# Kernel optimization log

Hardware: AMD Instinct MI355X
Metric: run time of the kernel (lower is better)

## Reference

```python
import jax, jax.numpy as jnp
import numpy as np
import math

C, HEADS = 128, 4
HD = C // HEADS
MID = max(C // 4, 8)

def _conv1x1(x, W, b):
    # x: (B?, C, H, W) ; W: (O, C) ; b: (O,)
    return jnp.einsum('bchw,oc->bohw', x, W) + b[None, :, None, None]

def _conv3x3(x, W, b):
    # W: (O, I, 3, 3), NCHW / OIHW, SAME padding
    y = jax.lax.conv_general_dilated(x, W, window_strides=(1, 1), padding='SAME',
                                     dimension_numbers=('NCHW', 'OIHW', 'NCHW'))
    return y + b[None, :, None, None]

def setup_inputs() -> dict:
    key = jax.random.key(0)
    ks = jax.random.split(key, 24)
    B, N, H, W = 4, 6, 128, 128
    s = 0.05
    inp = {
        'bev_views': jax.random.normal(ks[0], (B, N, C, H, W), jnp.float32),
        'snr_db': jax.random.normal(ks[1], (B, 1), jnp.float32) * 10.0,
        'view_reliability': jax.random.uniform(ks[2], (B, N, 3), jnp.float32),
        'Wq': jax.random.normal(ks[3], (C, C), jnp.float32) * s,
        'bq': jnp.zeros((C,), jnp.float32),
        'Wk': jax.random.normal(ks[4], (C, C), jnp.float32) * s,
        'bk': jnp.zeros((C,), jnp.float32),
        'Wv': jax.random.normal(ks[5], (C, C), jnp.float32) * s,
        'bv': jnp.zeros((C,), jnp.float32),
        'Wo1': jax.random.normal(ks[6], (C, C), jnp.float32) * s,
        'bo1': jnp.zeros((C,), jnp.float32),
        'Wo2': jax.random.normal(ks[7], (C, C, 3, 3), jnp.float32) * s,
        'bo2': jnp.zeros((C,), jnp.float32),
        'Wc1': jax.random.normal(ks[8], (MID, C), jnp.float32) * s,
        'bc1': jnp.zeros((MID,), jnp.float32),
        'Wc2': jax.random.normal(ks[9], (1, MID), jnp.float32) * s,
        'bc2': jnp.zeros((1,), jnp.float32),
        'Wg': jax.random.normal(ks[10], (C, 1), jnp.float32) * s,
        'bg': jnp.zeros((C,), jnp.float32),
        'Wr1': jax.random.normal(ks[11], (MID, 3), jnp.float32) * s,
        'br1': jnp.zeros((MID,), jnp.float32),
        'Wr2': jax.random.normal(ks[12], (1, MID), jnp.float32) * s,
        'br2': jnp.zeros((1,), jnp.float32),
    }
    return inp

def reference(bev_views, snr_db, view_reliability,
              Wq, bq, Wk, bk, Wv, bv, Wo1, bo1, Wo2, bo2,
              Wc1, bc1, Wc2, bc2, Wg, bg, Wr1, br1, Wr2, br2):
    B, N, Cc, H, W = bev_views.shape
    # --- cross-view semantic denoising (per-pixel cross-view attention) ---
    gq = bev_views.mean(axis=1)                       # (B,C,H,W)
    q = _conv1x1(gq, Wq, bq).reshape(B, HEADS, HD, H, W)
    flat = bev_views.reshape(B * N, Cc, H, W)
    k = _conv1x1(flat, Wk, bk).reshape(B, N, HEADS, HD, H, W)
    v = _conv1x1(flat, Wv, bv).reshape(B, N, HEADS, HD, H, W)
    # score over head_dim, softmax over views N
    score = jnp.einsum('bmdhw,bnmdhw->bnmhw', q, k) / math.sqrt(HD)
    attn = jax.nn.softmax(score, axis=1)              # (B,N,heads,H,W)
    fused = jnp.einsum('bnmhw,bnmdhw->bmdhw', attn, v).reshape(B, Cc, H, W)
    fused = _conv3x3(jax.nn.relu(_conv1x1(fused, Wo1, bo1)), Wo2, bo2) + gq
    attn_map = attn.mean(axis=2)                      # (B,N,H,W)
    # --- confidence-gated fusion ---
    conf = _conv1x1(jax.nn.relu(_conv1x1(flat, Wc1, bc1)), Wc2, bc2)
    conf_logits = conf.reshape(B, N, 1, H, W)
    rel_bias = (jax.nn.relu(view_reliability.reshape(B * N, 3) @ Wr1.T + br1) @ Wr2.T + br2)
    conf_logits = conf_logits + rel_bias.reshape(B, N, 1, 1, 1)
    conf_weights = jax.nn.softmax(conf_logits, axis=1)  # (B,N,1,H,W)
    fused_conf = (conf_weights * bev_views).sum(axis=1)  # (B,C,H,W)
    # --- SNR gate ---
    snr_norm = jnp.clip(snr_db / 20.0, -1.5, 1.5)       # (B,1)
    gate = jax.nn.sigmoid(snr_norm @ Wg.T + bg).reshape(B, Cc, 1, 1)
    out = gate * fused + (1.0 - gate) * fused_conf
    return (out, attn_map, conf_weights)
```

## Files before the change

### kernel.cpp

```cpp
#include <hip/hip_runtime.h>
#include <hip/hip_bf16.h>
#include <math.h>


#define BB   4
#define NV   6
#define CH   128
#define HGT  128
#define WID  128
#define MIDD 32
#define HWP  (HGT*WID)
#define TP   32

#define SWZ(pix) (((pix) & 15) << 3)

typedef __attribute__((ext_vector_type(8))) short bf16x8;
typedef __attribute__((ext_vector_type(4))) float f32x4;
typedef __attribute__((ext_vector_type(2))) unsigned int u32x2;

union U8 { bf16x8 v; unsigned u[4]; };

__device__ __forceinline__ ushort f2bf(float f) {
    union { __hip_bfloat16 h; ushort u; } v;
    v.h = __float2bfloat16(f);
    return v.u;
}
__device__ __forceinline__ float bf2f(ushort u) {
    return __uint_as_float(((unsigned)u) << 16);
}
__device__ __forceinline__ unsigned cvt_pk_bf16(float lo, float hi) {
    unsigned r;
    asm("v_cvt_pk_bf16_f32 %0, %1, %2" : "=v"(r) : "v"(lo), "v"(hi));
    return r;
}

__global__ void fusion_setup(const float* __restrict__ snr, const float* __restrict__ vr,
                             const float* __restrict__ Wg, const float* __restrict__ bg,
                             const float* __restrict__ Wr1, const float* __restrict__ br1,
                             const float* __restrict__ Wr2, const float* __restrict__ br2,
                             float* __restrict__ relb, float* __restrict__ gate)
{
    int tid = blockIdx.x * blockDim.x + threadIdx.x;
    if (tid < BB*CH) {
        int b = tid >> 7, c = tid & 127;
        float s = snr[b] * 0.05f;
        s = fminf(fmaxf(s, -1.5f), 1.5f);
        float z = s * Wg[c] + bg[c];
        gate[tid] = 1.0f / (1.0f + __expf(-z));
    }
    if (tid < BB*NV) {
        int b = tid / NV, n = tid % NV;
        float v0 = vr[(b*NV+n)*3+0], v1 = vr[(b*NV+n)*3+1], v2 = vr[(b*NV+n)*3+2];
        float acc = br2[0];
        for (int j = 0; j < MIDD; ++j) {
            float h = Wr1[j*3+0]*v0 + Wr1[j*3+1]*v1 + Wr1[j*3+2]*v2 + br1[j];
            acc += Wr2[j] * fmaxf(h, 0.0f);
        }
        relb[tid] = acc;
    }
}

__global__ void pack_weights(const float* __restrict__ Wq, const float* __restrict__ Wk,
                             const float* __restrict__ Wv, const float* __restrict__ Wo1,
                             const float* __restrict__ Wc1, const float* __restrict__ Wo2,
                             ushort* __restrict__ wqp, ushort* __restrict__ wkp,
                             ushort* __restrict__ wvp, ushort* __restrict__ wo1p,
                             ushort* __restrict__ wc1p, ushort* __restrict__ wo2p)
{
    int tid = blockIdx.x * 256 + threadIdx.x;
    if (tid >= 27136) return;
    if (tid < 8192) {
        int m = tid >> 11;
        int local = tid & 2047;
        const float* src = (m == 0) ? Wq : (m == 1) ? Wk : (m == 2) ? Wv : Wo1;
        ushort* dst = (m == 0) ? wqp : (m == 1) ? wkp : (m == 2) ? wvp : wo1p;
        int ks = local >> 9, rem = local & 511;
        int nf = rem >> 6, lane = rem & 63;
        int o = nf*16 + (lane & 15);
        int i0 = ks*32 + ((lane >> 4) << 3);
        const float* s = src + o*CH + i0;
        ushort* d = dst + local*8;
#pragma unroll
        for (int j = 0; j < 8; ++j) d[j] = f2bf(s[j]);
    } else if (tid < 8704) {
        int local = tid - 8192;
        int ks = local >> 7, rem = local & 127;
        int nf = rem >> 6, lane = rem & 63;
        int o = nf*16 + (lane & 15);
        int i0 = ks*32 + ((lane >> 4) << 3);
        const float* s = Wc1 + o*CH + i0;
        ushort* d = wc1p + local*8;
#pragma unroll
        for (int j = 0; j < 8; ++j) d[j] = f2bf(s[j]);
    } else {
        int l2 = tid - 8704;
        int lane = l2 & 63;
        int rest = l2 >> 6;
        int nf = rest & 7;
        int kst = rest >> 3;
        int ks = kst & 3;
        int tap = kst >> 2;
        int co = nf*16 + (lane & 15);
        int ci0 = ks*32 + ((lane >> 4) << 3);
        ushort* d = wo2p + l2*8;
#pragma unroll
        for (int j = 0; j < 8; ++j) d[j] = f2bf(Wo2[(co*CH + ci0 + j)*9 + tap]);
    }
}

__device__ __forceinline__ bf16x8 ldsA(const ushort* tile, int lane, int mf, int ks) {
    int pix = mf*16 + (lane & 15);
    int idx = (pix*128 + ks*32 + ((lane >> 4) << 3)) ^ SWZ(pix);
    return *(const bf16x8*)(tile + idx);
}
__device__ __forceinline__ bf16x8 ldB(const ushort* pack, int lane, int ks, int nf, int NF) {
    return *(const bf16x8*)(pack + (((ks*NF + nf)*64) + lane)*8);
}

__global__ __launch_bounds__(256, 3) void fusion_attn(
    const float* __restrict__ bev,
    const ushort* __restrict__ wqp, const ushort* __restrict__ wkp,
    const ushort* __restrict__ wvp, const ushort* __restrict__ wo1p,
    const ushort* __restrict__ wc1p,
    const float* __restrict__ bq, const float* __restrict__ bk,
    const float* __restrict__ bv, const float* __restrict__ bo1,
    const float* __restrict__ bc1, const float* __restrict__ bc2,
    const float* __restrict__ Wc2, const float* __restrict__ relb,
    ushort* __restrict__ gq_bf, ushort* __restrict__ t_bf, ushort* __restrict__ fc_bf,
    float* __restrict__ attn_o, float* __restrict__ conf_o)
{
    __shared__ ushort xt[NV][TP*128];
    __shared__ float  scat[NV][4][TP];
    __shared__ float  dnm[4][TP];
    __shared__ float  lpart[NV][TP];
    __shared__ float  cfw[NV][TP];

    const int t = threadIdx.x, lane = t & 63, w = t >> 6;
    const int vb = ((blockIdx.x & 7) << 8) | (blockIdx.x >> 3);
    const int b = vb >> 9;
    const int pix0 = (vb & 511) * TP;

    const int pixg = (t & 3) * 8;
    const int c0   = (t >> 2) * 2;
    const float* sb = bev + (((size_t)b*NV*CH + c0)*HWP + pix0 + pixg);
    const size_t vstep = (size_t)CH*HWP;
    float gacc[16];
#pragma unroll
    for (int i = 0; i < 16; ++i) gacc[i] = 0.f;
    float4 L[NV][4];
#pragma unroll
    for (int j = 0; j < NV; ++j) {
        const float* s1 = sb + (size_t)j*vstep;
        L[j][0] = *(const float4*)(s1);
        L[j][1] = *(const float4*)(s1 + 4);
        L[j][2] = *(const float4*)(s1 + HWP);
        L[j][3] = *(const float4*)(s1 + HWP + 4);
    }
#pragma unroll
    for (int n = 0; n < NV; ++n) {
        float4 a0 = L[n][0], a1 = L[n][1], b0 = L[n][2], b1 = L[n][3];
        float r0[8] = {a0.x,a0.y,a0.z,a0.w, a1.x,a1.y,a1.z,a1.w};
        float r1[8] = {b0.x,b0.y,b0.z,b0.w, b1.x,b1.y,b1.z,b1.w};
#pragma unroll
        for (int p = 0; p < 8; ++p) {
            int pix = pixg + p;
            unsigned pk = cvt_pk_bf16(r0[p], r1[p]);
            *(unsigned*)(&xt[n][(pix*128 + c0) ^ SWZ(pix)]) = pk;
            gacc[p]   += r0[p];
            gacc[8+p] += r1[p];
        }
    }
    {
        U8 g0, g1;
#pragma unroll
        for (int p = 0; p < 4; ++p) {
            g0.u[p] = cvt_pk_bf16(gacc[2*p]   * (1.0f/6.0f), gacc[2*p+1] * (1.0f/6.0f));
            g1.u[p] = cvt_pk_bf16(gacc[8+2*p] * (1.0f/6.0f), gacc[9+2*p] * (1.0f/6.0f));
        }
        ushort* gd = gq_bf + ((size_t)(b*CH + c0)*HWP + pix0 + pixg);
        *(bf16x8*)(gd)       = g0.v;
        *(bf16x8*)(gd + HWP) = g1.v;
    }
    __syncthreads();

    const int cl0 = (lane & 15);
    const int rg  = (lane >> 4) << 2;

    f32x4 qf[2][2];
#pragma unroll
    for (int mf = 0; mf < 2; ++mf)
#pragma unroll
        for (int nfl = 0; nfl < 2; ++nfl) qf[mf][nfl] = (f32x4){0.f,0.f,0.f,0.f};
#pragma unroll 2
    for (int n = 0; n < NV; ++n) {
        bf16x8 xA[2][4];
#pragma unroll
        for (int mf = 0; mf < 2; ++mf)
#pragma unroll
            for (int ks = 0; ks < 4; ++ks) xA[mf][ks] = ldsA(xt[n], lane, mf, ks);
#pragma unroll
        for (int nfl = 0; nfl < 2; ++nfl) {
#pragma unroll
            for (int ks = 0; ks < 4; ++ks) {
                bf16x8 bb = ldB(wqp, lane, ks, 2*w + nfl, 8);
#pragma unroll
                for (int mf = 0; mf < 2; ++mf)
                    qf[mf][nfl] = __builtin_amdgcn_mfma_f32_16x16x32_bf16(bb, xA[mf][ks], qf[mf][nfl], 0, 0, 0);
            }
        }
        if (n == w || n == w + 4) {
            f32x4 cf[2][2];
#pragma unroll
            for (int mf = 0; mf < 2; ++mf)
#pragma unroll
                for (int nfc = 0; nfc < 2; ++nfc) cf[mf][nfc] = (f32x4){0.f,0.f,0.f,0.f};
#pragma unroll
            for (int nfc = 0; nfc < 2; ++nfc) {
#pragma unroll
                for (int ks = 0; ks < 4; ++ks) {
                    bf16x8 bb = ldB(wc1p, lane, ks, nfc, 2);
#pragma unroll
                    for (int mf = 0; mf < 2; ++mf)
                        cf[mf][nfc] = __builtin_amdgcn_mfma_f32_16x16x32_bf16(bb, xA[mf][ks], cf[mf][nfc], 0, 0, 0);
                }
            }
            const f32x4 bc1T0 = *(const f32x4*)(bc1 + rg),  bc1T1 = *(const f32x4*)(bc1 + 16 + rg);
            const f32x4 wc2T0 = *(const f32x4*)(Wc2 + rg),  wc2T1 = *(const f32x4*)(Wc2 + 16 + rg);
#pragma unroll
            for (int mf = 0; mf < 2; ++mf) {
                float pl = 0.f;
#pragma unroll
                for (int r = 0; r < 4; ++r) {
                    pl += fmaxf(cf[mf][0][r] + bc1T0[r], 0.f) * wc2T0[r];
                    pl += fmaxf(cf[mf][1][r] + bc1T1[r], 0.f) * wc2T1[r];
                }
                pl += __shfl_xor(pl, 16, 64);
                pl += __shfl_xor(pl, 32, 64);
                if (lane < 16) lpart[n][mf*16 + lane] = pl;
            }
        }
    }
    {
        const f32x4 bqT0 = *(const f32x4*)(bq + w*32 + rg), bqT1 = *(const f32x4*)(bq + w*32 + 16 + rg);
#pragma unroll
        for (int mf = 0; mf < 2; ++mf)
#pragma unroll
            for (int r = 0; r < 4; ++r) {
                qf[mf][0][r] = qf[mf][0][r]*(1.0f/6.0f) + bqT0[r];
                qf[mf][1][r] = qf[mf][1][r]*(1.0f/6.0f) + bqT1[r];
            }
    }

    float sb2[2];
    {
        const f32x4 bkT0 = *(const f32x4*)(bk + w*32 + rg), bkT1 = *(const f32x4*)(bk + w*32 + 16 + rg);
#pragma unroll
        for (int mf = 0; mf < 2; ++mf) {
            float v = 0.f;
#pragma unroll
            for (int r = 0; r < 4; ++r) {
                v += qf[mf][0][r]*bkT0[r];
                v += qf[mf][1][r]*bkT1[r];
            }
            sb2[mf] = v;
        }
    }
    float denom[2] = {0.f, 0.f};
#pragma unroll 2
    for (int n = 0; n < NV; ++n) {
        bf16x8 xA[2][4];
#pragma unroll
        for (int mf = 0; mf < 2; ++mf)
#pragma unroll
            for (int ks = 0; ks < 4; ++ks) xA[mf][ks] = ldsA(xt[n], lane, mf, ks);
        f32x4 kf[2][2];
#pragma unroll
        for (int mf = 0; mf < 2; ++mf)
#pragma unroll
            for (int nfl = 0; nfl < 2; ++nfl) kf[mf][nfl] = (f32x4){0.f,0.f,0.f,0.f};
#pragma unroll
        for (int nfl = 0; nfl < 2; ++nfl)
#pragma unroll
            for (int ks = 0; ks < 4; ++ks) {
                bf16x8 bb = ldB(wkp, lane, ks, 2*w + nfl, 8);
#pragma unroll
                for (int mf = 0; mf < 2; ++mf)
                    kf[mf][nfl] = __builtin_amdgcn_mfma_f32_16x16x32_bf16(bb, xA[mf][ks], kf[mf][nfl], 0, 0, 0);
            }
#pragma unroll
        for (int mf = 0; mf < 2; ++mf) {
            float s = sb2[mf];
#pragma unroll
            for (int r = 0; r < 4; ++r) {
                s += qf[mf][0][r]*kf[mf][0][r];
                s += qf[mf][1][r]*kf[mf][1][r];
            }
            s += __shfl_xor(s, 16, 64);
            s += __shfl_xor(s, 32, 64);
            float e = __expf(s * 0.17677669529663687f);
            denom[mf] += e;
            if (lane < 16) scat[n][w][mf*16 + lane] = e;
        }
    }
    const float inv0 = 1.0f/denom[0], inv1 = 1.0f/denom[1];
    if (lane < 32) dnm[w][lane] = (lane & 16) ? inv1 : inv0;

    f32x4 ff[2][2];
#pragma unroll
    for (int mf = 0; mf < 2; ++mf)
#pragma unroll
        for (int nfl = 0; nfl < 2; ++nfl) ff[mf][nfl] = (f32x4){0.f,0.f,0.f,0.f};
#pragma unroll 2
    for (int n = 0; n < NV; ++n) {
        bf16x8 xA[2][4];
#pragma unroll
        for (int mf = 0; mf < 2; ++mf)
#pragma unroll
            for (int ks = 0; ks < 4; ++ks) xA[mf][ks] = ldsA(xt[n], lane, mf, ks);
        f32x4 vv[2][2];
#pragma unroll
        for (int mf = 0; mf < 2; ++mf)
#pragma unroll
            for (int nfl = 0; nfl < 2; ++nfl) vv[mf][nfl] = (f32x4){0.f,0.f,0.f,0.f};
#pragma unroll
        for (int nfl = 0; nfl < 2; ++nfl)
#pragma unroll
            for (int ks = 0; ks < 4; ++ks) {
                bf16x8 bb = ldB(wvp, lane, ks, 2*w + nfl, 8);
#pragma unroll
                for (int mf = 0; mf < 2; ++mf)
                    vv[mf][nfl] = __builtin_amdgcn_mfma_f32_16x16x32_bf16(bb, xA[mf][ks], vv[mf][nfl], 0, 0, 0);
            }
        float a0 = scat[n][w][cl0]      * inv0;
        float a1 = scat[n][w][16 + cl0] * inv1;
#pragma unroll
        for (int r = 0; r < 4; ++r) {
            ff[0][0][r] += a0 * vv[0][0][r];
            ff[0][1][r] += a0 * vv[0][1][r];
            ff[1][0][r] += a1 * vv[1][0][r];
            ff[1][1][r] += a1 * vv[1][1][r];
        }
    }
    {
        const f32x4 bvT0 = *(const f32x4*)(bv + w*32 + rg), bvT1 = *(const f32x4*)(bv + w*32 + 16 + rg);
#pragma unroll
        for (int mf = 0; mf < 2; ++mf)
#pragma unroll
            for (int r = 0; r < 4; ++r) { ff[mf][0][r] += bvT0[r]; ff[mf][1][r] += bvT1[r]; }
    }
    __syncthreads();

    if (t < 32) {
        int pix = t;
        float bc2v = bc2[0];
        float lg[NV];
#pragma unroll
        for (int n = 0; n < NV; ++n)
            lg[n] = lpart[n][pix] + bc2v + relb[b*NV + n];
        float mx = fmaxf(fmaxf(fmaxf(lg[0],lg[1]),fmaxf(lg[2],lg[3])),fmaxf(lg[4],lg[5]));
        float e[NV], sum = 0.f;
#pragma unroll
        for (int n = 0; n < NV; ++n) { e[n] = __expf(lg[n]-mx); sum += e[n]; }
        float inv = 1.0f/sum;
#pragma unroll
        for (int n = 0; n < NV; ++n) {
            float wv = e[n]*inv;
            cfw[n][pix] = wv;
            conf_o[(b*NV + n)*HWP + pix0 + pix] = wv;
        }
    }
    if (t < 192) {
        int n = t >> 5, pix = t & 31;
        float am = 0.25f*(scat[n][0][pix]*dnm[0][pix] + scat[n][1][pix]*dnm[1][pix]
                        + scat[n][2][pix]*dnm[2][pix] + scat[n][3][pix]*dnm[3][pix]);
        attn_o[(b*NV + n)*HWP + pix0 + pix] = am;
    }
    __syncthreads();

    {
        float fcv[16];
#pragma unroll
        for (int i = 0; i < 16; ++i) fcv[i] = 0.f;
#pragma unroll
        for (int n = 0; n < NV; ++n) {
#pragma unroll
            for (int p = 0; p < 8; ++p) {
                int pix = pixg + p;
                float cwv = cfw[n][pix];
                unsigned pk = *(const unsigned*)(&xt[n][(pix*128 + c0) ^ SWZ(pix)]);
                fcv[p]   += cwv * bf2f((ushort)(pk & 0xffffu));
                fcv[8+p] += cwv * bf2f((ushort)(pk >> 16));
            }
        }
        U8 f0, f1;
#pragma unroll
        for (int p = 0; p < 4; ++p) {
            f0.u[p] = cvt_pk_bf16(fcv[2*p],   fcv[2*p+1]);
            f1.u[p] = cvt_pk_bf16(fcv[8+2*p], fcv[9+2*p]);
        }
        ushort* fd = fc_bf + ((size_t)(b*CH + c0)*HWP + pix0 + pixg);
        *(bf16x8*)(fd)       = f0.v;
        *(bf16x8*)(fd + HWP) = f1.v;
    }
    __syncthreads();

    {
        ushort* xt0 = &xt[0][0];
#pragma unroll
        for (int mf = 0; mf < 2; ++mf)
#pragma unroll
            for (int nfl = 0; nfl < 2; ++nfl) {
                int pix = mf*16 + cl0;
                int c   = w*32 + nfl*16 + rg;
                unsigned lo = cvt_pk_bf16(ff[mf][nfl][0], ff[mf][nfl][1]);
                unsigned hi = cvt_pk_bf16(ff[mf][nfl][2], ff[mf][nfl][3]);
                *(u32x2*)(&xt0[(pix*128 + c) ^ SWZ(pix)]) = (u32x2){lo, hi};
            }
    }
    __syncthreads();

    {
        bf16x8 aA[2][4];
#pragma unroll
        for (int mf = 0; mf < 2; ++mf)
#pragma unroll
            for (int ks = 0; ks < 4; ++ks) aA[mf][ks] = ldsA(&xt[0][0], lane, mf, ks);
        f32x4 tf[2][2];
#pragma unroll
        for (int mf = 0; mf < 2; ++mf)
#pragma unroll
            for (int nfl = 0; nfl < 2; ++nfl) tf[mf][nfl] = (f32x4){0.f,0.f,0.f,0.f};
#pragma unroll
        for (int nfl = 0; nfl < 2; ++nfl) {
            int nf = 2*w + nfl;
#pragma unroll
            for (int ks = 0; ks < 4; ++ks) {
                bf16x8 bb = ldB(wo1p, lane, ks, nf, 8);
#pragma unroll
                for (int mf = 0; mf < 2; ++mf)
                    tf[mf][nfl] = __builtin_amdgcn_mfma_f32_16x16x32_bf16(aA[mf][ks], bb, tf[mf][nfl], 0, 0, 0);
            }
        }
        const float bov0 = bo1[w*32 + cl0], bov1 = bo1[w*32 + 16 + cl0];
#pragma unroll
        for (int mf = 0; mf < 2; ++mf)
#pragma unroll
            for (int nfl = 0; nfl < 2; ++nfl)
#pragma unroll
                for (int r = 0; r < 4; ++r) {
                    int pix = mf*16 + rg + r;
                    int c   = w*32 + nfl*16 + cl0;
                    float bo_ = nfl ? bov1 : bov0;
                    t_bf[(size_t)(b*HWP + pix0 + pix)*128 + c] = f2bf(fmaxf(tf[mf][nfl][r] + bo_, 0.f));
                }
    }
}

__global__ __launch_bounds__(256, 1) void fusion_conv3(
    const ushort* __restrict__ t_bf, const ushort* __restrict__ gq_bf,
    const ushort* __restrict__ fc_bf, const ushort* __restrict__ wo2p,
    const float* __restrict__ bo2, const float* __restrict__ gate,
    float* __restrict__ out)
{
    __shared__ ushort halo[2][18*18*64];

    const int t = threadIdx.x, lane = t & 63, w = t >> 6;
    const int b = blockIdx.x >> 6;
    const int tile = blockIdx.x & 63;
    const int h0 = (tile >> 3) * 16;
    const int w0 = (tile & 7) * 16;

    const int c8   = (t & 7) * 8;
    const int cell0 = t >> 3;

    for (int i = cell0; i < 324; i += 32) {
        int r = i / 18, cc = i - r*18;
        int hs = h0 - 1 + r, wsr = w0 - 1 + cc;
        bf16x8 v = (bf16x8){0,0,0,0,0,0,0,0};
        if ((unsigned)hs < (unsigned)HGT && (unsigned)wsr < (unsigned)WID)
            v = *(const bf16x8*)(t_bf + ((size_t)(b*HWP + hs*WID + wsr)*128 + c8));
        *(bf16x8*)(&halo[0][(i*64 + c8) ^ ((cc & 7) << 3)]) = v;
    }
    bf16x8 stg[11];
#pragma unroll
    for (int j = 0; j < 11; ++j) {
        int i = cell0 + 32*j;
        if (i < 324) {
            int r = i / 18, cc = i - r*18;
            int hs = h0 - 1 + r, wsr = w0 - 1 + cc;
            bf16x8 v = (bf16x8){0,0,0,0,0,0,0,0};
            if ((unsigned)hs < (unsigned)HGT && (unsigned)wsr < (unsigned)WID)
                v = *(const bf16x8*)(t_bf + ((size_t)(b*HWP + hs*WID + wsr)*128 + 64 + c8));
            stg[j] = v;
        }
    }
    __syncthreads();

    f32x4 acc[4][8];
#pragma unroll
    for (int mi = 0; mi < 4; ++mi)
#pragma unroll
        for (int nf = 0; nf < 8; ++nf) acc[mi][nf] = (f32x4){0.f,0.f,0.f,0.f};

    const int mcol = lane & 15;
    const int koff = (lane >> 4) << 3;

#pragma unroll 1
    for (int k = 0; k < 2; ++k) {
#pragma unroll 1
        for (int tap = 0; tap < 9; ++tap) {
            const int dy = tap / 3, dx = tap - dy*3;
            const int col = mcol + dx;
            const int swz = (col & 7) << 3;
#pragma unroll
            for (int ks2 = 0; ks2 < 2; ++ks2) {
                bf16x8 Bf[8];
#pragma unroll
                for (int nf = 0; nf < 8; ++nf)
                    Bf[nf] = *(const bf16x8*)(wo2p + (((size_t)((tap*4 + k*2 + ks2)*8 + nf))*64 + lane)*8);
#pragma unroll
                for (int mi = 0; mi < 4; ++mi) {
                    int mf = w*4 + mi;
                    int idx = (((mf + dy)*18 + col)*64 + ks2*32 + koff) ^ swz;
                    bf16x8 Af = *(const bf16x8*)(&halo[k][idx]);
#pragma unroll
                    for (int nf = 0; nf < 8; ++nf)
                        acc[mi][nf] = __builtin_amdgcn_mfma_f32_16x16x32_bf16(Af, Bf[nf], acc[mi][nf], 0, 0, 0);
                }
            }
        }
        if (k == 0) {
#pragma unroll
            for (int j = 0; j < 11; ++j) {
                int i = cell0 + 32*j;
                if (i < 324) {
                    int cc = i % 18;
                    *(bf16x8*)(&halo[1][(i*64 + c8) ^ ((cc & 7) << 3)]) = stg[j];
                }
            }
            __syncthreads();
        }
    }
    __syncthreads();

    float* fbuf = (float*)halo;
    const int cl0 = lane & 15;
    const int rg  = (lane >> 4) << 2;
    const int c_l = t & 63;
    const int rgw = (t >> 6) * 4;
#pragma unroll 1
    for (int nfg = 0; nfg < 2; ++nfg) {
#pragma unroll
        for (int mi = 0; mi < 4; ++mi)
#pragma unroll
            for (int nl = 0; nl < 4; ++nl) {
                int nf = nfg*4 + nl;
                int pix = (w*4 + mi)*16 + rg;
                *(f32x4*)(fbuf + (nl*16 + cl0)*260 + pix) = acc[mi][nf];
            }
        __syncthreads();
        {
            const int c  = nfg*64 + c_l;
            const float gt  = gate[b*CH + c];
            const float gti = 1.0f - gt;
            const float b2v = bo2[c];
#pragma unroll
            for (int rr = 0; rr < 4; ++rr) {
                int row = rgw + rr;
                const int gbase = (b*CH + c)*HWP + (h0 + row)*WID + w0;
                float vv[16];
#pragma unroll
                for (int q = 0; q < 2; ++q) {
                    f32x4 cv0 = *(const f32x4*)(fbuf + c_l*260 + row*16 + q*8);
                    f32x4 cv1 = *(const f32x4*)(fbuf + c_l*260 + row*16 + q*8 + 4);
                    bf16x8 gq8 = *(const bf16x8*)(gq_bf + gbase + q*8);
                    bf16x8 fc8 = *(const bf16x8*)(fc_bf + gbase + q*8);
#pragma unroll
                    for (int jj = 0; jj < 4; ++jj) {
                        vv[q*8+jj]   = gt*(cv0[jj] + b2v + bf2f((ushort)gq8[jj]))   + gti*bf2f((ushort)fc8[jj]);
                        vv[q*8+4+jj] = gt*(cv1[jj] + b2v + bf2f((ushort)gq8[4+jj])) + gti*bf2f((ushort)fc8[4+jj]);
                    }
                }
                float* od = out + gbase;
                *(float4*)(od)      = (float4){vv[0],vv[1],vv[2],vv[3]};
                *(float4*)(od + 4)  = (float4){vv[4],vv[5],vv[6],vv[7]};
                *(float4*)(od + 8)  = (float4){vv[8],vv[9],vv[10],vv[11]};
                *(float4*)(od + 12) = (float4){vv[12],vv[13],vv[14],vv[15]};
            }
        }
        __syncthreads();
    }
}

extern "C" void kernel_launch(void* const* d_in, const int* in_sizes, int n_in,
                              void* d_out, int out_size, void* d_ws, size_t ws_size,
                              hipStream_t stream)
{
    const float* bev = (const float*)d_in[0];
    const float* snr = (const float*)d_in[1];
    const float* vr  = (const float*)d_in[2];
    const float* Wq  = (const float*)d_in[3];
    const float* bq  = (const float*)d_in[4];
    const float* Wk  = (const float*)d_in[5];
    const float* bk  = (const float*)d_in[6];
    const float* Wv  = (const float*)d_in[7];
    const float* bv  = (const float*)d_in[8];
    const float* Wo1 = (const float*)d_in[9];
    const float* bo1 = (const float*)d_in[10];
    const float* Wo2 = (const float*)d_in[11];
    const float* bo2 = (const float*)d_in[12];
    const float* Wc1 = (const float*)d_in[13];
    const float* bc1 = (const float*)d_in[14];
    const float* Wc2 = (const float*)d_in[15];
    const float* bc2 = (const float*)d_in[16];
    const float* Wg  = (const float*)d_in[17];
    const float* bg  = (const float*)d_in[18];
    const float* Wr1 = (const float*)d_in[19];
    const float* br1 = (const float*)d_in[20];
    const float* Wr2 = (const float*)d_in[21];
    const float* br2 = (const float*)d_in[22];

    char* wsb = (char*)d_ws;
    ushort* t_bf  = (ushort*)(wsb);
    ushort* gq_bf = (ushort*)(wsb + 16777216);
    ushort* fc_bf = (ushort*)(wsb + 33554432);
    ushort* wqp   = (ushort*)(wsb + 50331648);
    ushort* wkp   = wqp + 16384;
    ushort* wvp   = wkp + 16384;
    ushort* wo1p  = wvp + 16384;
    ushort* wc1p  = wo1p + 16384;
    ushort* wo2p  = wc1p + 4096;
    float*  gate  = (float*)(wsb + 50331648 + 434176);
    float*  relb  = gate + 512;

    float* outp   = (float*)d_out;
    float* attn_o = outp + 8388608;
    float* conf_o = outp + 8781824;

    fusion_setup<<<2, 256, 0, stream>>>(snr, vr, Wg, bg, Wr1, br1, Wr2, br2,
                                        relb, gate);
    pack_weights<<<106, 256, 0, stream>>>(Wq, Wk, Wv, Wo1, Wc1, Wo2,
                                          wqp, wkp, wvp, wo1p, wc1p, wo2p);
    fusion_attn<<<2048, 256, 0, stream>>>(bev, wqp, wkp, wvp, wo1p, wc1p,
                                          bq, bk, bv, bo1, bc1, bc2, Wc2, relb,
                                          gq_bf, t_bf, fc_bf, attn_o, conf_o);
    fusion_conv3<<<256, 256, 0, stream>>>(t_bf, gq_bf, fc_bf, wo2p, bo2, gate, outp);
}
```

Measured before the change: 162.6 us.

## Split conv3x3 output channels across two blocks and single-buffer the halo

The 3x3 conv kernel now launches 512 blocks, each computing half of the output channels, where it used to launch 256 blocks covering all 128 channels. The halo buffer in shared memory drops from double to single buffering, with an extra barrier before the second channel-half overwrite. Halving the LDS footprint and accumulator registers allows two blocks per CU, raising occupancy and filling more of the GPU's CUs. In exchange, each halo tile is loaded twice from global memory, once per channel group.

```diff
diff --git a/kernel.cpp b/kernel.cpp
--- a/kernel.cpp
+++ b/kernel.cpp
@@ -456,17 +456,18 @@
     }
 }
 
-__global__ __launch_bounds__(256, 1) void fusion_conv3(
+__global__ __launch_bounds__(256, 2) void fusion_conv3(
     const ushort* __restrict__ t_bf, const ushort* __restrict__ gq_bf,
     const ushort* __restrict__ fc_bf, const ushort* __restrict__ wo2p,
     const float* __restrict__ bo2, const float* __restrict__ gate,
     float* __restrict__ out)
 {
-    __shared__ ushort halo[2][18*18*64];
+    __shared__ ushort halo[18*18*64];
 
     const int t = threadIdx.x, lane = t & 63, w = t >> 6;
-    const int b = blockIdx.x >> 6;
-    const int tile = blockIdx.x & 63;
+    const int cg   = blockIdx.x & 1;
+    const int tile = (blockIdx.x >> 1) & 63;
+    const int b    = blockIdx.x >> 7;
     const int h0 = (tile >> 3) * 16;
     const int w0 = (tile & 7) * 16;
 
@@ -479,7 +480,7 @@
         bf16x8 v = (bf16x8){0,0,0,0,0,0,0,0};
         if ((unsigned)hs < (unsigned)HGT && (unsigned)wsr < (unsigned)WID)
             v = *(const bf16x8*)(t_bf + ((size_t)(b*HWP + hs*WID + wsr)*128 + c8));
-        *(bf16x8*)(&halo[0][(i*64 + c8) ^ ((cc & 7) << 3)]) = v;
+        *(bf16x8*)(&halo[(i*64 + c8) ^ ((cc & 7) << 3)]) = v;
     }
     bf16x8 stg[11];
 #pragma unroll
@@ -496,11 +497,11 @@
     }
     __syncthreads();
 
-    f32x4 acc[4][8];
+    f32x4 acc[4][4];
 #pragma unroll
     for (int mi = 0; mi < 4; ++mi)
 #pragma unroll
-        for (int nf = 0; nf < 8; ++nf) acc[mi][nf] = (f32x4){0.f,0.f,0.f,0.f};
+        for (int nfl = 0; nfl < 4; ++nfl) acc[mi][nfl] = (f32x4){0.f,0.f,0.f,0.f};
 
     const int mcol = lane & 15;
     const int koff = (lane >> 4) << 3;
@@ -514,65 +515,66 @@
             const int swz = (col & 7) << 3;
 #pragma unroll
             for (int ks2 = 0; ks2 < 2; ++ks2) {
-                bf16x8 Bf[8];
-#pragma unroll
-                for (int nf = 0; nf < 8; ++nf)
-                    Bf[nf] = *(const bf16x8*)(wo2p + (((size_t)((tap*4 + k*2 + ks2)*8 + nf))*64 + lane)*8);
+                bf16x8 Bf[4];
+#pragma unroll
+                for (int nfl = 0; nfl < 4; ++nfl)
+                    Bf[nfl] = *(const bf16x8*)(wo2p + (((size_t)((tap*4 + k*2 + ks2)*8 + cg*4 + nfl))*64 + lane)*8);
 #pragma unroll
                 for (int mi = 0; mi < 4; ++mi) {
                     int mf = w*4 + mi;
                     int idx = (((mf + dy)*18 + col)*64 + ks2*32 + koff) ^ swz;
-                    bf16x8 Af = *(const bf16x8*)(&halo[k][idx]);
-#pragma unroll
-                    for (int nf = 0; nf < 8; ++nf)
-                        acc[mi][nf] = __builtin_amdgcn_mfma_f32_16x16x32_bf16(Af, Bf[nf], acc[mi][nf], 0, 0, 0);
+                    bf16x8 Af = *(const bf16x8*)(&halo[idx]);
+#pragma unroll
+                    for (int nfl = 0; nfl < 4; ++nfl)
+                        acc[mi][nfl] = __builtin_amdgcn_mfma_f32_16x16x32_bf16(Af, Bf[nfl], acc[mi][nfl], 0, 0, 0);
                 }
             }
         }
         if (k == 0) {
+            __syncthreads();
 #pragma unroll
             for (int j = 0; j < 11; ++j) {
                 int i = cell0 + 32*j;
                 if (i < 324) {
                     int cc = i % 18;
-                    *(bf16x8*)(&halo[1][(i*64 + c8) ^ ((cc & 7) << 3)]) = stg[j];
+                    *(bf16x8*)(&halo[(i*64 + c8) ^ ((cc & 7) << 3)]) = stg[j];
                 }
             }
             __syncthreads();
         }
     }
-    __syncthreads();
 
     float* fbuf = (float*)halo;
     const int cl0 = lane & 15;
     const int rg  = (lane >> 4) << 2;
-    const int c_l = t & 63;
-    const int rgw = (t >> 6) * 4;
+    const int c32 = t & 31;
+    const int rowg = (t >> 5) * 2;
 #pragma unroll 1
-    for (int nfg = 0; nfg < 2; ++nfg) {
+    for (int sp = 0; sp < 2; ++sp) {
+        __syncthreads();
 #pragma unroll
         for (int mi = 0; mi < 4; ++mi)
 #pragma unroll
-            for (int nl = 0; nl < 4; ++nl) {
-                int nf = nfg*4 + nl;
+            for (int nl = 0; nl < 2; ++nl) {
+                int nfl = sp*2 + nl;
                 int pix = (w*4 + mi)*16 + rg;
-                *(f32x4*)(fbuf + (nl*16 + cl0)*260 + pix) = acc[mi][nf];
+                *(f32x4*)(fbuf + (nl*16 + cl0)*260 + pix) = acc[mi][nfl];
             }
         __syncthreads();
         {
-            const int c  = nfg*64 + c_l;
+            const int c  = cg*64 + sp*32 + c32;
             const float gt  = gate[b*CH + c];
             const float gti = 1.0f - gt;
             const float b2v = bo2[c];
 #pragma unroll
-            for (int rr = 0; rr < 4; ++rr) {
-                int row = rgw + rr;
+            for (int rr = 0; rr < 2; ++rr) {
+                int row = rowg + rr;
                 const int gbase = (b*CH + c)*HWP + (h0 + row)*WID + w0;
                 float vv[16];
 #pragma unroll
                 for (int q = 0; q < 2; ++q) {
-                    f32x4 cv0 = *(const f32x4*)(fbuf + c_l*260 + row*16 + q*8);
-                    f32x4 cv1 = *(const f32x4*)(fbuf + c_l*260 + row*16 + q*8 + 4);
+                    f32x4 cv0 = *(const f32x4*)(fbuf + c32*260 + row*16 + q*8);
+                    f32x4 cv1 = *(const f32x4*)(fbuf + c32*260 + row*16 + q*8 + 4);
                     bf16x8 gq8 = *(const bf16x8*)(gq_bf + gbase + q*8);
                     bf16x8 fc8 = *(const bf16x8*)(fc_bf + gbase + q*8);
 #pragma unroll
@@ -588,7 +590,6 @@
                 *(float4*)(od + 12) = (float4){vv[12],vv[13],vv[14],vv[15]};
             }
         }
-        __syncthreads();
     }
 }
 
@@ -644,5 +645,5 @@
     fusion_attn<<<2048, 256, 0, stream>>>(bev, wqp, wkp, wvp, wo1p, wc1p,
                                           bq, bk, bv, bo1, bc1, bc2, Wc2, relb,
                                           gq_bf, t_bf, fc_bf, attn_o, conf_o);
-    fusion_conv3<<<256, 256, 0, stream>>>(t_bf, gq_bf, fc_bf, wo2p, bo2, gate, outp);
-}
+    fusion_conv3<<<512, 256, 0, stream>>>(t_bf, gq_bf, fc_bf, wo2p, bo2, gate, outp);
+}
```

Result: faster. 158.8 us (-2.4%).
